# Kernel optimization log

Measured on AMD Instinct MI355X. Metric: run time of the kernel, lower is better.

## Reference

```python
import jax, jax.numpy as jnp
import numpy as np

B, S, D, DOUT = 16, 1024, 768, 256
TEMP = D ** 0.5


def setup_inputs() -> dict:
    key = jax.random.key(0)
    ks = jax.random.split(key, 16)
    emb = jax.random.normal(ks[0], (B, S, D), dtype=jnp.float32)
    mask = jax.random.randint(ks[1], (B, S), 0, 2, dtype=jnp.int32)
    scale = 0.02
    def lin(kw, kb, din, dout):
        return (jax.random.normal(kw, (din, dout), dtype=jnp.float32) * scale,
                jax.random.normal(kb, (dout,), dtype=jnp.float32) * scale)
    q_Wq, q_bq = lin(ks[2], ks[3], D, D)
    q_Wk, q_bk = lin(ks[4], ks[5], D, D)
    q_Wv, q_bv = lin(ks[6], ks[7], D, DOUT)
    d_Wq, d_bq = lin(ks[8], ks[9], D, D)
    d_Wk, d_bk = lin(ks[10], ks[11], D, D)
    d_Wv, d_bv = lin(ks[12], ks[13], D, DOUT)
    return {
        'emb': emb, 'mask': mask, 'is_query': 1,
        'query_Wq': q_Wq, 'query_bq': q_bq,
        'query_Wk': q_Wk, 'query_bk': q_bk,
        'query_Wv': q_Wv, 'query_bv': q_bv,
        'doc_Wq': d_Wq, 'doc_bq': d_bq,
        'doc_Wk': d_Wk, 'doc_bk': d_bk,
        'doc_Wv': d_Wv, 'doc_bv': d_bv,
    }


def reference(emb, mask, is_query,
              query_Wq, query_bq, query_Wk, query_bk, query_Wv, query_bv,
              doc_Wq, doc_bq, doc_Wk, doc_bk, doc_Wv, doc_bv):
    # is_query is a static Python int/bool selecting the projection set
    if is_query:
        Wq, bq, Wk, bk, Wv, bv = query_Wq, query_bq, query_Wk, query_bk, query_Wv, query_bv
    else:
        Wq, bq, Wk, bk, Wv, bv = doc_Wq, doc_bq, doc_Wk, doc_bk, doc_Wv, doc_bv
    q = jnp.einsum('bsd,de->bse', emb, Wq) + bq  # [B,S,D]
    k = jnp.einsum('bsd,de->bse', emb, Wk) + bk  # [B,S,D]
    v = jnp.einsum('bsd,de->bse', emb, Wv) + bv  # [B,S,DOUT]
    attn = jnp.einsum('bqd,bkd->bqk', q / TEMP, k)  # [B,S,S]
    attn = jnp.where(mask[:, None, :] == 0, jnp.float32(-1e9), attn)
    attn = jax.nn.softmax(attn, axis=-1)
    out = jnp.einsum('bqk,bkd->bqd', attn, v)  # [B,S,DOUT]
    return out, attn
```

## Files before the change

### kernel.cpp

```cpp
#include <hip/hip_runtime.h>
#include <hip/hip_bf16.h>

static constexpr float INV_TEMP = 0.03608439182435161f;

typedef __attribute__((ext_vector_type(8))) short bf16x8;
typedef __attribute__((ext_vector_type(4))) float f32x4;
typedef __attribute__((ext_vector_type(8))) unsigned short u16x8;
typedef __attribute__((ext_vector_type(4))) unsigned short u16x4;

__device__ __forceinline__ unsigned short f2bf(float f) {
  unsigned u = __float_as_uint(f);
  u += 0x7fffu + ((u >> 16) & 1u);
  return (unsigned short)(u >> 16);
}
__device__ __forceinline__ float bf2f(unsigned short h) {
  return __uint_as_float((unsigned)h << 16);
}

__device__ __forceinline__ void async_copy16(const void* g, void* lds) {
  __builtin_amdgcn_global_load_lds(
      (const __attribute__((address_space(1))) unsigned int*)g,
      (__attribute__((address_space(3))) unsigned int*)lds, 16, 0, 0);
}

__global__ __launch_bounds__(256) void pack_emb(const float* __restrict__ src,
                                                unsigned short* __restrict__ dst) {
  long i = ((long)blockIdx.x * 256 + threadIdx.x) * 8;
  float4 a = *(const float4*)(src + i);
  float4 b = *(const float4*)(src + i + 4);
  u16x8 v;
  v[0] = f2bf(a.x); v[1] = f2bf(a.y); v[2] = f2bf(a.z); v[3] = f2bf(a.w);
  v[4] = f2bf(b.x); v[5] = f2bf(b.y); v[6] = f2bf(b.z); v[7] = f2bf(b.w);
  *(u16x8*)(dst + i) = v;
}

__global__ __launch_bounds__(256) void pack_sel(
    const int* __restrict__ isq_p,
    const float* qWq, const float* qWk, const float* qWv, const float* qbv,
    const float* dWq, const float* dWk, const float* dWv, const float* dbv,
    unsigned short* __restrict__ Wq_bf,
    unsigned short* __restrict__ Wk_bf,
    unsigned short* __restrict__ WvT,
    float* __restrict__ bias_v) {
  const int b = blockIdx.x, t = threadIdx.x;
  const int isq = *isq_p;
  if (b < 1152) {
    const int which = b >= 576;
    const float* W = which ? (isq ? qWk : dWk) : (isq ? qWq : dWq);
    unsigned short* o = which ? Wk_bf : Wq_bf;
    const long i = ((long)(which ? b - 576 : b) * 256 + t) * 4;
    float4 x = *(const float4*)(W + i);
    u16x4 y; y[0] = f2bf(x.x); y[1] = f2bf(x.y); y[2] = f2bf(x.z); y[3] = f2bf(x.w);
    *(u16x4*)(o + i) = y;
  } else if (b < 1344) {
    const float* Wv = isq ? qWv : dWv;
    const long base = ((long)(b - 1152) * 256 + t) * 4;
#pragma unroll
    for (int j = 0; j < 4; ++j) {
      long o = base + j;
      int n = (int)(o / 768), d = (int)(o % 768);
      WvT[o] = f2bf(Wv[(long)d * 256 + n]);
    }
  } else {
    const float* bv = isq ? qbv : dbv;
    if (t < 256) bias_v[t] = bv[t];
  }
}

__global__ __launch_bounds__(256) void gemm_g(
    const unsigned short* __restrict__ Wk_bf,
    const unsigned short* __restrict__ Wq_bf,
    unsigned short* __restrict__ Gt) {
  __shared__ unsigned short Ab[2][64 * 32];
  __shared__ unsigned short Bb[2][64 * 32];
  const int tid = threadIdx.x, wid = tid >> 6, lane = tid & 63;
  const unsigned short* A = Wk_bf + (long)blockIdx.x * 64 * 768;
  const unsigned short* BT = Wq_bf + (long)blockIdx.y * 64 * 768;

  auto stage = [&](int buf, int kt) {
    const int e = tid * 8, row = e >> 5, col = e & 31;
    async_copy16(A + (long)row * 768 + kt * 32 + col, &Ab[buf][e]);
    async_copy16(BT + (long)row * 768 + kt * 32 + col, &Bb[buf][e]);
  };

  f32x4 acc[2][2] = {};
  stage(0, 0);
  __syncthreads();
  int buf = 0;
  const int wr = wid >> 1, wc = wid & 1;
  const int fr = lane & 15, fq = lane >> 4;
  for (int kt = 0; kt < 24; ++kt) {
    if (kt + 1 < 24) stage(buf ^ 1, kt + 1);
    const unsigned short* Ap = &Ab[buf][(wr * 32 + fr) * 32 + fq * 8];
    const unsigned short* Bp = &Bb[buf][(wc * 32 + fr) * 32 + fq * 8];
    bf16x8 a[2], b[2];
#pragma unroll
    for (int mi = 0; mi < 2; ++mi) a[mi] = *(const bf16x8*)(Ap + mi * 16 * 32);
#pragma unroll
    for (int ni = 0; ni < 2; ++ni) b[ni] = *(const bf16x8*)(Bp + ni * 16 * 32);
#pragma unroll
    for (int mi = 0; mi < 2; ++mi)
#pragma unroll
      for (int ni = 0; ni < 2; ++ni)
        acc[mi][ni] = __builtin_amdgcn_mfma_f32_16x16x32_bf16(a[mi], b[ni], acc[mi][ni], 0, 0, 0);
    __syncthreads();
    buf ^= 1;
  }
#pragma unroll
  for (int mi = 0; mi < 2; ++mi)
#pragma unroll
    for (int ni = 0; ni < 2; ++ni) {
      const long m = (long)blockIdx.x * 64 + wr * 32 + mi * 16 + fq * 4;
      const long n = (long)blockIdx.y * 64 + wc * 32 + ni * 16 + fr;
      f32x4 v = acc[mi][ni];
#pragma unroll
      for (int r = 0; r < 4; ++r) Gt[(m + r) * 768 + n] = f2bf(v[r]);
    }
}

__global__ __launch_bounds__(256) void uvc_fast(
    const int* __restrict__ isq_p,
    const float* qWq, const float* qbq, const float* qWk, const float* qbk,
    const float* dWq, const float* dbq, const float* dWk, const float* dbk,
    unsigned short* __restrict__ Gt, float* __restrict__ bias_t) {
  const int b = blockIdx.x, t = threadIdx.x;
  const int isq = *isq_p;
  const float* Wq = isq ? qWq : dWq;  const float* bq = isq ? qbq : dbq;
  const float* Wk = isq ? qWk : dWk;  const float* bk = isq ? qbk : dbk;
  __shared__ float red[256];
  if (b < 1536) {
    const int lo = (b < 768);
    const int d = lo ? b : b - 768;
    const float* W = lo ? Wq : Wk;
    const float* bvec = lo ? bk : bq;
    float s = 0.f;
#pragma unroll
    for (int i = 0; i < 3; ++i) {
      const int a = t + i * 256;
      s += W[(long)d * 768 + a] * bvec[a];
    }
    red[t] = s;
    __syncthreads();
    for (int off = 128; off; off >>= 1) {
      if (t < off) red[t] += red[t + off];
      __syncthreads();
    }
    if (t == 0) Gt[(long)(lo ? 768 : 769) * 768 + d] = f2bf(red[0]);
  } else {
    for (int i = t; i < 1024; i += 256) bias_t[i] = 0.f;
    float p = 0.f;
    for (int a = t; a < 768; a += 256) p += bq[a] * bk[a];
    red[t] = p;
    __syncthreads();
    for (int off = 128; off; off >>= 1) {
      if (t < off) red[t] += red[t + off];
      __syncthreads();
    }
    if (t == 0) bias_t[768] = red[0];
  }
}

__device__ __forceinline__ void k_loop_256(
    const unsigned short* __restrict__ Apan, long lda,
    const unsigned short* __restrict__ Bpan, long ldb,
    int nk, unsigned short* smem, f32x4 (&acc)[8][4]) {
  const int tid = threadIdx.x;
  const int wid = tid >> 6, lane = tid & 63;
  const int wr = wid >> 2, wc = wid & 3;
  const int fr = lane & 15, fq = lane >> 4;

  auto stage = [&](int tile, int mat, int ks, int buf) {
    const unsigned short* g = (mat ? Bpan : Apan) + (long)tile * 64 + ks * 32;
    const long ld = mat ? ldb : lda;
    unsigned short* d = smem + (((buf << 2) | (mat << 1) | ks) << 13);
#pragma unroll
    for (int i = 0; i < 2; ++i) {
      const int e = (tid + i * 512) * 8;
      const int row = e >> 5;
      const int sl = (e >> 3) & 3;
      const int ss = sl ^ ((row >> 1) & 3);
      async_copy16(g + (long)row * ld + ss * 8, d + e);
    }
  };

  const int fro = fr * 32 + ((fq ^ ((fr >> 1) & 3)) << 3);
  const int awo = fro + (wr * 128) * 32;
  const int bwo = fro + (wc * 64) * 32;

  stage(0, 0, 0, 0); stage(0, 1, 0, 0); stage(0, 0, 1, 0); stage(0, 1, 1, 0);
  if (nk > 1) {
    stage(1, 0, 0, 1); stage(1, 1, 1, 1);
    asm volatile("s_waitcnt vmcnt(4)" ::: "memory");
  } else {
    asm volatile("s_waitcnt vmcnt(0)" ::: "memory");
  }
  __builtin_amdgcn_sched_barrier(0);
  __builtin_amdgcn_s_barrier();

  for (int t = 0; t < nk; ++t) {
    const int p = t & 1;
    const unsigned short* A0 = smem + (((p << 2) | 0) << 13);
    const unsigned short* A1 = smem + (((p << 2) | 1) << 13);
    const unsigned short* B0 = smem + (((p << 2) | 2) << 13);
    const unsigned short* B1 = smem + (((p << 2) | 3) << 13);
    bf16x8 a[4], b[4];

#pragma unroll
    for (int m = 0; m < 4; ++m) a[m] = *(const bf16x8*)(A0 + awo + m * 512);
#pragma unroll
    for (int n = 0; n < 4; ++n) b[n] = *(const bf16x8*)(B0 + bwo + n * 512);
    if (t + 1 < nk) stage(t + 1, 0, 1, (t + 1) & 1);
    __builtin_amdgcn_s_barrier();
    asm volatile("s_waitcnt lgkmcnt(0)");
    __builtin_amdgcn_sched_barrier(0);
    __builtin_amdgcn_s_setprio(1);
#pragma unroll
    for (int m = 0; m < 4; ++m)
#pragma unroll
      for (int n = 0; n < 4; ++n)
        acc[m][n] = __builtin_amdgcn_mfma_f32_16x16x32_bf16(a[m], b[n], acc[m][n], 0, 0, 0);
    __builtin_amdgcn_s_setprio(0);
    __builtin_amdgcn_sched_barrier(0);
    __builtin_amdgcn_s_barrier();

#pragma unroll
    for (int m = 0; m < 4; ++m) a[m] = *(const bf16x8*)(A0 + awo + (4 + m) * 512);
    if (t + 1 < nk) stage(t + 1, 1, 0, (t + 1) & 1);
    __builtin_amdgcn_s_barrier();
    asm volatile("s_waitcnt lgkmcnt(0)");
    __builtin_amdgcn_sched_barrier(0);
    __builtin_amdgcn_s_setprio(1);
#pragma unroll
    for (int m = 0; m < 4; ++m)
#pragma unroll
      for (int n = 0; n < 4; ++n)
        acc[4 + m][n] = __builtin_amdgcn_mfma_f32_16x16x32_bf16(a[m], b[n], acc[4 + m][n], 0, 0, 0);
    __builtin_amdgcn_s_setprio(0);
    __builtin_amdgcn_sched_barrier(0);
    __builtin_amdgcn_s_barrier();

#pragma unroll
    for (int m = 0; m < 4; ++m) a[m] = *(const bf16x8*)(A1 + awo + m * 512);
#pragma unroll
    for (int n = 0; n < 4; ++n) b[n] = *(const bf16x8*)(B1 + bwo + n * 512);
    if (t + 2 < nk) stage(t + 2, 0, 0, p);
    __builtin_amdgcn_s_barrier();
    asm volatile("s_waitcnt lgkmcnt(0)");
    __builtin_amdgcn_sched_barrier(0);
    __builtin_amdgcn_s_setprio(1);
#pragma unroll
    for (int m = 0; m < 4; ++m)
#pragma unroll
      for (int n = 0; n < 4; ++n)
        acc[m][n] = __builtin_amdgcn_mfma_f32_16x16x32_bf16(a[m], b[n], acc[m][n], 0, 0, 0);
    __builtin_amdgcn_s_setprio(0);
    __builtin_amdgcn_sched_barrier(0);
    __builtin_amdgcn_s_barrier();

#pragma unroll
    for (int m = 0; m < 4; ++m) a[m] = *(const bf16x8*)(A1 + awo + (4 + m) * 512);
    if (t + 2 < nk) stage(t + 2, 1, 1, p);
    __builtin_amdgcn_s_barrier();
    asm volatile("s_waitcnt lgkmcnt(0)");
    __builtin_amdgcn_sched_barrier(0);
    __builtin_amdgcn_s_setprio(1);
#pragma unroll
    for (int m = 0; m < 4; ++m)
#pragma unroll
      for (int n = 0; n < 4; ++n)
        acc[4 + m][n] = __builtin_amdgcn_mfma_f32_16x16x32_bf16(a[m], b[n], acc[4 + m][n], 0, 0, 0);
    __builtin_amdgcn_s_setprio(0);
    if (t < nk - 2) {
      asm volatile("s_waitcnt vmcnt(4)" ::: "memory");
    } else if (t == nk - 2) {
      asm volatile("s_waitcnt vmcnt(0)" ::: "memory");
    }
    __builtin_amdgcn_sched_barrier(0);
    __builtin_amdgcn_s_barrier();
  }
}

__global__ __launch_bounds__(512, 2) void tproj256(
    const unsigned short* __restrict__ emb_bf,
    const unsigned short* __restrict__ Gt,
    const float* __restrict__ bias_t,
    unsigned short* __restrict__ T) {
  extern __shared__ unsigned short smem[];
  const int f = blockIdx.x;
  const int kx = f & 7, c = f >> 3;
  const long bx = 8 * kx + (c & 7);
  const long yb = c >> 3;
  const unsigned short* Apan = emb_bf + bx * 256 * 768;
  const unsigned short* Bpan = Gt + yb * 256 * 768;
  f32x4 acc[8][4];
#pragma unroll
  for (int m = 0; m < 8; ++m)
#pragma unroll
    for (int n = 0; n < 4; ++n) acc[m][n] = f32x4{0.f, 0.f, 0.f, 0.f};

  k_loop_256(Apan, 768, Bpan, 768, 12, smem, acc);

  const int wid = threadIdx.x >> 6, lane = threadIdx.x & 63;
  const int wr = wid >> 2, wc = wid & 3;
  const int fr = lane & 15, fq = lane >> 4;
#pragma unroll
  for (int m = 0; m < 8; ++m)
#pragma unroll
    for (int n = 0; n < 4; ++n) {
      const long mm = bx * 256 + wr * 128 + m * 16 + fq * 4;
      const long nn = yb * 256 + wc * 64 + n * 16 + fr;
      const float bb = bias_t[nn];
      f32x4 v = acc[m][n];
#pragma unroll
      for (int r = 0; r < 4; ++r) T[(mm + r) * 1024 + nn] = f2bf(v[r] + bb);
    }
}

__global__ __launch_bounds__(512, 2) void logits256(
    const unsigned short* __restrict__ T,
    const unsigned short* __restrict__ emb_bf,
    float* __restrict__ attn) {
  extern __shared__ unsigned short smem[];
  const int f = blockIdx.x;
  const int kx = f & 7, c = f >> 3;
  const int bz = 2 * kx + (c >> 4);
  const int inner = c & 15, bx = inner & 3, by = inner >> 2;
  const unsigned short* Tb = T + (long)bz * 1024 * 1024;
  const unsigned short* Apan = Tb + (long)bx * 256 * 1024;
  const unsigned short* Bpan = emb_bf + (long)bz * 1024 * 768 + (long)by * 256 * 768;
  f32x4 acc[8][4];
#pragma unroll
  for (int m = 0; m < 8; ++m)
#pragma unroll
    for (int n = 0; n < 4; ++n) acc[m][n] = f32x4{0.f, 0.f, 0.f, 0.f};

  k_loop_256(Apan, 1024, Bpan, 768, 12, smem, acc);

  const int wid = threadIdx.x >> 6, lane = threadIdx.x & 63;
  const int wr = wid >> 2, wc = wid & 3;
  const int fr = lane & 15, fq = lane >> 4;
  float* C = attn + (long)bz * 1024 * 1024;
#pragma unroll
  for (int m = 0; m < 8; ++m)
#pragma unroll
    for (int n = 0; n < 4; ++n) {
      const long mm = (long)bx * 256 + wr * 128 + m * 16 + fq * 4;
      const long nn = (long)by * 256 + wc * 64 + n * 16 + fr;
      const float cB = bf2f(Tb[nn * 1024 + 769]);
      f32x4 v = acc[m][n];
#pragma unroll
      for (int r = 0; r < 4; ++r) {
        const float rA = bf2f(Tb[(mm + r) * 1024 + 768]);
        C[(mm + r) * 1024 + nn] = (v[r] + rA + cB) * INV_TEMP;
      }
    }
}

__global__ __launch_bounds__(256) void gemm_vt(
    const unsigned short* __restrict__ WvT,
    const unsigned short* __restrict__ emb_bf,
    const float* __restrict__ bias_v,
    unsigned short* __restrict__ VT) {
  __shared__ unsigned short Ab[2][128 * 32];
  __shared__ unsigned short Bb[2][128 * 32];
  const int tid = threadIdx.x, wid = tid >> 6, lane = tid & 63;
  const unsigned short* A = WvT + (long)blockIdx.x * 128 * 768;
  const unsigned short* BT = emb_bf + (long)blockIdx.y * 128 * 768;
  const int srow = lane >> 2;
  const int skk = (lane & 3) * 8;

  auto stage = [&](int buf, int kt) {
    const unsigned short* As = A + (long)kt * 32;
    const unsigned short* Bs = BT + (long)kt * 32;
#pragma unroll
    for (int i = 0; i < 2; ++i) {
      int c = wid * 2 + i;
      async_copy16(As + (long)(c * 16 + srow) * 768 + skk, &Ab[buf][c * 512]);
      async_copy16(Bs + (long)(c * 16 + srow) * 768 + skk, &Bb[buf][c * 512]);
    }
  };

  f32x4 acc[4][4] = {};
  stage(0, 0);
  __syncthreads();
  int buf = 0;
  const int wr = wid >> 1, wc = wid & 1;
  const int fr = lane & 15, fq = lane >> 4;
  for (int kt = 0; kt < 24; ++kt) {
    if (kt + 1 < 24) stage(buf ^ 1, kt + 1);
    const unsigned short* Ap = &Ab[buf][(wr * 64 + fr) * 32 + fq * 8];
    const unsigned short* Bp = &Bb[buf][(wc * 64 + fr) * 32 + fq * 8];
    bf16x8 af[4], bfv[4];
#pragma unroll
    for (int mi = 0; mi < 4; ++mi) af[mi] = *(const bf16x8*)(Ap + mi * 16 * 32);
#pragma unroll
    for (int ni = 0; ni < 4; ++ni) bfv[ni] = *(const bf16x8*)(Bp + ni * 16 * 32);
#pragma unroll
    for (int mi = 0; mi < 4; ++mi)
#pragma unroll
      for (int ni = 0; ni < 4; ++ni)
        acc[mi][ni] = __builtin_amdgcn_mfma_f32_16x16x32_bf16(af[mi], bfv[ni], acc[mi][ni], 0, 0, 0);
    __syncthreads();
    buf ^= 1;
  }
#pragma unroll
  for (int mi = 0; mi < 4; ++mi)
#pragma unroll
    for (int ni = 0; ni < 4; ++ni) {
      const long m = (long)blockIdx.x * 128 + wr * 64 + mi * 16 + fq * 4;
      const long n = (long)blockIdx.y * 128 + wc * 64 + ni * 16 + fr;
      f32x4 v = acc[mi][ni];
#pragma unroll
      for (int r = 0; r < 4; ++r)
        VT[(m + r) * 16384 + n] = f2bf(v[r] + bias_v[m + r]);
    }
}

__global__ __launch_bounds__(256) void softmax_rows(float* __restrict__ attn,
                                                    const int* __restrict__ mask,
                                                    unsigned short* __restrict__ attn_bf) {
  const int row = blockIdx.x;
  const int b = row >> 10;
  float* p = attn + (long)row * 1024;
  const int tid = threadIdx.x, lane = tid & 63, wid = tid >> 6;
  float4 v = ((const float4*)p)[tid];
  int4 mk = ((const int4*)(mask + b * 1024))[tid];
  v.x = mk.x ? v.x : -1e9f;
  v.y = mk.y ? v.y : -1e9f;
  v.z = mk.z ? v.z : -1e9f;
  v.w = mk.w ? v.w : -1e9f;
  float mx = fmaxf(fmaxf(v.x, v.y), fmaxf(v.z, v.w));
#pragma unroll
  for (int off = 32; off; off >>= 1) mx = fmaxf(mx, __shfl_xor(mx, off));
  __shared__ float red[4];
  if (lane == 0) red[wid] = mx;
  __syncthreads();
  mx = fmaxf(fmaxf(red[0], red[1]), fmaxf(red[2], red[3]));
  float e0 = __expf(v.x - mx), e1 = __expf(v.y - mx);
  float e2 = __expf(v.z - mx), e3 = __expf(v.w - mx);
  float s = e0 + e1 + e2 + e3;
#pragma unroll
  for (int off = 32; off; off >>= 1) s += __shfl_xor(s, off);
  __shared__ float red2[4];
  if (lane == 0) red2[wid] = s;
  __syncthreads();
  s = red2[0] + red2[1] + red2[2] + red2[3];
  const float inv = 1.0f / s;
  float4 o;
  o.x = e0 * inv; o.y = e1 * inv; o.z = e2 * inv; o.w = e3 * inv;
  ((float4*)p)[tid] = o;
  u16x4 ob;
  ob[0] = f2bf(o.x); ob[1] = f2bf(o.y); ob[2] = f2bf(o.z); ob[3] = f2bf(o.w);
  *(u16x4*)(attn_bf + (long)row * 1024 + tid * 4) = ob;
}

__global__ __launch_bounds__(256) void gemm_pv(
    const unsigned short* __restrict__ attnbf,
    const unsigned short* __restrict__ VT,
    float* __restrict__ out) {
  __shared__ unsigned short Ab[2][128 * 32];
  __shared__ unsigned short Bb[2][64 * 32];
  const int tid = threadIdx.x, wid = tid >> 6, lane = tid & 63;
  const int bz = blockIdx.z;
  const unsigned short* A = attnbf + (long)bz * 1024 * 1024 + (long)blockIdx.x * 128 * 1024;
  const unsigned short* BT = VT + (long)bz * 1024 + (long)blockIdx.y * 64 * 16384;
  const int srow = lane >> 2;
  const int skk = (lane & 3) * 8;

  auto stage = [&](int buf, int kt) {
    const unsigned short* As = A + (long)kt * 32;
    const unsigned short* Bs = BT + (long)kt * 32;
#pragma unroll
    for (int i = 0; i < 2; ++i) {
      int c = wid * 2 + i;
      async_copy16(As + (long)(c * 16 + srow) * 1024 + skk, &Ab[buf][c * 512]);
    }
    async_copy16(Bs + (long)(wid * 16 + srow) * 16384 + skk, &Bb[buf][wid * 512]);
  };

  f32x4 acc[4][2] = {};
  stage(0, 0);
  __syncthreads();
  int buf = 0;
  const int wr = wid >> 1, wc = wid & 1;
  const int fr = lane & 15, fq = lane >> 4;
  for (int kt = 0; kt < 32; ++kt) {
    if (kt + 1 < 32) stage(buf ^ 1, kt + 1);
    const unsigned short* Ap = &Ab[buf][(wr * 64 + fr) * 32 + fq * 8];
    const unsigned short* Bp = &Bb[buf][(wc * 32 + fr) * 32 + fq * 8];
    bf16x8 af[4], bfv[2];
#pragma unroll
    for (int mi = 0; mi < 4; ++mi) af[mi] = *(const bf16x8*)(Ap + mi * 16 * 32);
#pragma unroll
    for (int ni = 0; ni < 2; ++ni) bfv[ni] = *(const bf16x8*)(Bp + ni * 16 * 32);
#pragma unroll
    for (int mi = 0; mi < 4; ++mi)
#pragma unroll
      for (int ni = 0; ni < 2; ++ni)
        acc[mi][ni] = __builtin_amdgcn_mfma_f32_16x16x32_bf16(af[mi], bfv[ni], acc[mi][ni], 0, 0, 0);
    __syncthreads();
    buf ^= 1;
  }

  float* C = out + (long)bz * 1024 * 256;
  const long m0 = (long)blockIdx.x * 128 + wr * 64;
  const long n0 = (long)blockIdx.y * 64 + wc * 32;
#pragma unroll
  for (int mi = 0; mi < 4; ++mi)
#pragma unroll
    for (int ni = 0; ni < 2; ++ni) {
      const long m = m0 + mi * 16 + fq * 4;
      const long n = n0 + ni * 16 + fr;
      f32x4 v = acc[mi][ni];
#pragma unroll
      for (int r = 0; r < 4; ++r) C[(m + r) * 256 + n] = v[r];
    }
}

extern "C" void kernel_launch(void* const* d_in, const int* in_sizes, int n_in,
                              void* d_out, int out_size, void* d_ws, size_t ws_size,
                              hipStream_t stream) {
  const float* emb = (const float*)d_in[0];
  const int* mask = (const int*)d_in[1];
  const int* isq = (const int*)d_in[2];
  const float* qWq = (const float*)d_in[3];  const float* qbq = (const float*)d_in[4];
  const float* qWk = (const float*)d_in[5];  const float* qbk = (const float*)d_in[6];
  const float* qWv = (const float*)d_in[7];  const float* qbv = (const float*)d_in[8];
  const float* dWq = (const float*)d_in[9];  const float* dbq = (const float*)d_in[10];
  const float* dWk = (const float*)d_in[11]; const float* dbk = (const float*)d_in[12];
  const float* dWv = (const float*)d_in[13]; const float* dbv = (const float*)d_in[14];

  char* ws = (char*)d_ws;
  unsigned short* emb_bf = (unsigned short*)ws;  ws += (size_t)16384 * 768 * 2;
  unsigned short* Wq_bf  = (unsigned short*)ws;  ws += (size_t)768 * 768 * 2;
  unsigned short* Wk_bf  = (unsigned short*)ws;  ws += (size_t)768 * 768 * 2;
  unsigned short* WvT    = (unsigned short*)ws;  ws += (size_t)256 * 768 * 2;
  unsigned short* Gt     = (unsigned short*)ws;  ws += (size_t)1024 * 768 * 2;
  float*          bias_v = (float*)ws;           ws += (size_t)256 * 4;
  float*          bias_t = (float*)ws;           ws += (size_t)1024 * 4;
  unsigned short* T      = (unsigned short*)ws;  ws += (size_t)16384 * 1024 * 2;
  unsigned short* VT     = (unsigned short*)ws;  ws += (size_t)256 * 16384 * 2;
  unsigned short* attnbf = (unsigned short*)ws;  ws += (size_t)16 * 1024 * 1024 * 2;

  float* out = (float*)d_out;
  float* attn = out + (size_t)16 * 1024 * 256;

  (void)hipFuncSetAttribute((const void*)&tproj256,
                            hipFuncAttributeMaxDynamicSharedMemorySize, 131072);
  (void)hipFuncSetAttribute((const void*)&logits256,
                            hipFuncAttributeMaxDynamicSharedMemorySize, 131072);

  hipLaunchKernelGGL(pack_emb, dim3(6144), dim3(256), 0, stream, emb, emb_bf);
  hipLaunchKernelGGL(pack_sel, dim3(1345), dim3(256), 0, stream, isq,
                     qWq, qWk, qWv, qbv, dWq, dWk, dWv, dbv, Wq_bf, Wk_bf, WvT, bias_v);
  hipLaunchKernelGGL(gemm_g, dim3(12, 12), dim3(256), 0, stream, Wk_bf, Wq_bf, Gt);
  hipLaunchKernelGGL(uvc_fast, dim3(1537), dim3(256), 0, stream, isq,
                     qWq, qbq, qWk, qbk, dWq, dbq, dWk, dbk, Gt, bias_t);
  hipLaunchKernelGGL(tproj256, dim3(256), dim3(512), 131072, stream,
                     emb_bf, Gt, bias_t, T);
  hipLaunchKernelGGL(gemm_vt, dim3(2, 128), dim3(256), 0, stream,
                     WvT, emb_bf, bias_v, VT);
  hipLaunchKernelGGL(logits256, dim3(256), dim3(512), 131072, stream,
                     T, emb_bf, attn);
  hipLaunchKernelGGL(softmax_rows, dim3(16384), dim3(256), 0, stream, attn, mask, attnbf);
  hipLaunchKernelGGL(gemm_pv, dim3(8, 4, 16), dim3(256), 0, stream, attnbf, VT, out);
}
```

Measured before the change: 171.9 us.

## Move rank-1 bias terms from padded T projection into extended V projection

The two bias-derived vectors (emb·Wq·bk and emb·Wk·bq) are now produced as extra rows of the V projection instead of as extra padded columns of the T = emb·G projection. T shrinks from 1024 to 768 columns, so the tproj GEMM launches 192 blocks instead of 256 and writes less data. The logits epilogue now reads the row and column bias vectors from the extended VT buffer. In exchange, gemm_vt grows from 2 to 3 row tiles, most of which is padding computed from uninitialized weight rows and never read.

```diff
diff --git a/kernel.cpp b/kernel.cpp
--- a/kernel.cpp
+++ b/kernel.cpp
@@ -40,7 +40,7 @@
     const float* dWq, const float* dWk, const float* dWv, const float* dbv,
     unsigned short* __restrict__ Wq_bf,
     unsigned short* __restrict__ Wk_bf,
-    unsigned short* __restrict__ WvT,
+    unsigned short* __restrict__ WvTe,
     float* __restrict__ bias_v) {
   const int b = blockIdx.x, t = threadIdx.x;
   const int isq = *isq_p;
@@ -59,7 +59,7 @@
     for (int j = 0; j < 4; ++j) {
       long o = base + j;
       int n = (int)(o / 768), d = (int)(o % 768);
-      WvT[o] = f2bf(Wv[(long)d * 256 + n]);
+      WvTe[o] = f2bf(Wv[(long)d * 256 + n]);
     }
   } else {
     const float* bv = isq ? qbv : dbv;
@@ -122,7 +122,7 @@
     const int* __restrict__ isq_p,
     const float* qWq, const float* qbq, const float* qWk, const float* qbk,
     const float* dWq, const float* dbq, const float* dWk, const float* dbk,
-    unsigned short* __restrict__ Gt, float* __restrict__ bias_t) {
+    unsigned short* __restrict__ WvTe, float* __restrict__ bias_v) {
   const int b = blockIdx.x, t = threadIdx.x;
   const int isq = *isq_p;
   const float* Wq = isq ? qWq : dWq;  const float* bq = isq ? qbq : dbq;
@@ -145,9 +145,9 @@
       if (t < off) red[t] += red[t + off];
       __syncthreads();
     }
-    if (t == 0) Gt[(long)(lo ? 768 : 769) * 768 + d] = f2bf(red[0]);
+    if (t == 0) WvTe[(long)(lo ? 256 : 257) * 768 + d] = f2bf(red[0]);
   } else {
-    for (int i = t; i < 1024; i += 256) bias_t[i] = 0.f;
+    if (t < 128) bias_v[256 + t] = 0.f;
     float p = 0.f;
     for (int a = t; a < 768; a += 256) p += bq[a] * bk[a];
     red[t] = p;
@@ -156,7 +156,7 @@
       if (t < off) red[t] += red[t + off];
       __syncthreads();
     }
-    if (t == 0) bias_t[768] = red[0];
+    if (t == 0) bias_v[256] = red[0];
   }
 }
 
@@ -283,7 +283,6 @@
 __global__ __launch_bounds__(512, 2) void tproj256(
     const unsigned short* __restrict__ emb_bf,
     const unsigned short* __restrict__ Gt,
-    const float* __restrict__ bias_t,
     unsigned short* __restrict__ T) {
   extern __shared__ unsigned short smem[];
   const int f = blockIdx.x;
@@ -309,24 +308,23 @@
     for (int n = 0; n < 4; ++n) {
       const long mm = bx * 256 + wr * 128 + m * 16 + fq * 4;
       const long nn = yb * 256 + wc * 64 + n * 16 + fr;
-      const float bb = bias_t[nn];
       f32x4 v = acc[m][n];
 #pragma unroll
-      for (int r = 0; r < 4; ++r) T[(mm + r) * 1024 + nn] = f2bf(v[r] + bb);
+      for (int r = 0; r < 4; ++r) T[(mm + r) * 768 + nn] = f2bf(v[r]);
     }
 }
 
 __global__ __launch_bounds__(512, 2) void logits256(
     const unsigned short* __restrict__ T,
     const unsigned short* __restrict__ emb_bf,
+    const unsigned short* __restrict__ VTe,
     float* __restrict__ attn) {
   extern __shared__ unsigned short smem[];
   const int f = blockIdx.x;
   const int kx = f & 7, c = f >> 3;
   const int bz = 2 * kx + (c >> 4);
   const int inner = c & 15, bx = inner & 3, by = inner >> 2;
-  const unsigned short* Tb = T + (long)bz * 1024 * 1024;
-  const unsigned short* Apan = Tb + (long)bx * 256 * 1024;
+  const unsigned short* Apan = T + (long)bz * 1024 * 768 + (long)bx * 256 * 768;
   const unsigned short* Bpan = emb_bf + (long)bz * 1024 * 768 + (long)by * 256 * 768;
   f32x4 acc[8][4];
 #pragma unroll
@@ -334,37 +332,39 @@
 #pragma unroll
     for (int n = 0; n < 4; ++n) acc[m][n] = f32x4{0.f, 0.f, 0.f, 0.f};
 
-  k_loop_256(Apan, 1024, Bpan, 768, 12, smem, acc);
+  k_loop_256(Apan, 768, Bpan, 768, 12, smem, acc);
 
   const int wid = threadIdx.x >> 6, lane = threadIdx.x & 63;
   const int wr = wid >> 2, wc = wid & 3;
   const int fr = lane & 15, fq = lane >> 4;
   float* C = attn + (long)bz * 1024 * 1024;
+  const unsigned short* rvec = VTe + (long)256 * 16384 + (long)bz * 1024;
+  const unsigned short* cvec = VTe + (long)257 * 16384 + (long)bz * 1024;
 #pragma unroll
   for (int m = 0; m < 8; ++m)
 #pragma unroll
     for (int n = 0; n < 4; ++n) {
       const long mm = (long)bx * 256 + wr * 128 + m * 16 + fq * 4;
       const long nn = (long)by * 256 + wc * 64 + n * 16 + fr;
-      const float cB = bf2f(Tb[nn * 1024 + 769]);
+      const float cB = bf2f(cvec[nn]);
       f32x4 v = acc[m][n];
 #pragma unroll
       for (int r = 0; r < 4; ++r) {
-        const float rA = bf2f(Tb[(mm + r) * 1024 + 768]);
+        const float rA = bf2f(rvec[mm + r]);
         C[(mm + r) * 1024 + nn] = (v[r] + rA + cB) * INV_TEMP;
       }
     }
 }
 
 __global__ __launch_bounds__(256) void gemm_vt(
-    const unsigned short* __restrict__ WvT,
+    const unsigned short* __restrict__ WvTe,
     const unsigned short* __restrict__ emb_bf,
     const float* __restrict__ bias_v,
-    unsigned short* __restrict__ VT) {
+    unsigned short* __restrict__ VTe) {
   __shared__ unsigned short Ab[2][128 * 32];
   __shared__ unsigned short Bb[2][128 * 32];
   const int tid = threadIdx.x, wid = tid >> 6, lane = tid & 63;
-  const unsigned short* A = WvT + (long)blockIdx.x * 128 * 768;
+  const unsigned short* A = WvTe + (long)blockIdx.x * 128 * 768;
   const unsigned short* BT = emb_bf + (long)blockIdx.y * 128 * 768;
   const int srow = lane >> 2;
   const int skk = (lane & 3) * 8;
@@ -412,7 +412,7 @@
       f32x4 v = acc[mi][ni];
 #pragma unroll
       for (int r = 0; r < 4; ++r)
-        VT[(m + r) * 16384 + n] = f2bf(v[r] + bias_v[m + r]);
+        VTe[(m + r) * 16384 + n] = f2bf(v[r] + bias_v[m + r]);
     }
 }
 
@@ -456,14 +456,14 @@
 
 __global__ __launch_bounds__(256) void gemm_pv(
     const unsigned short* __restrict__ attnbf,
-    const unsigned short* __restrict__ VT,
+    const unsigned short* __restrict__ VTe,
     float* __restrict__ out) {
   __shared__ unsigned short Ab[2][128 * 32];
   __shared__ unsigned short Bb[2][64 * 32];
   const int tid = threadIdx.x, wid = tid >> 6, lane = tid & 63;
   const int bz = blockIdx.z;
   const unsigned short* A = attnbf + (long)bz * 1024 * 1024 + (long)blockIdx.x * 128 * 1024;
-  const unsigned short* BT = VT + (long)bz * 1024 + (long)blockIdx.y * 64 * 16384;
+  const unsigned short* BT = VTe + (long)bz * 1024 + (long)blockIdx.y * 64 * 16384;
   const int srow = lane >> 2;
   const int skk = (lane & 3) * 8;
 
@@ -534,12 +534,11 @@
   unsigned short* emb_bf = (unsigned short*)ws;  ws += (size_t)16384 * 768 * 2;
   unsigned short* Wq_bf  = (unsigned short*)ws;  ws += (size_t)768 * 768 * 2;
   unsigned short* Wk_bf  = (unsigned short*)ws;  ws += (size_t)768 * 768 * 2;
-  unsigned short* WvT    = (unsigned short*)ws;  ws += (size_t)256 * 768 * 2;
-  unsigned short* Gt     = (unsigned short*)ws;  ws += (size_t)1024 * 768 * 2;
-  float*          bias_v = (float*)ws;           ws += (size_t)256 * 4;
-  float*          bias_t = (float*)ws;           ws += (size_t)1024 * 4;
-  unsigned short* T      = (unsigned short*)ws;  ws += (size_t)16384 * 1024 * 2;
-  unsigned short* VT     = (unsigned short*)ws;  ws += (size_t)256 * 16384 * 2;
+  unsigned short* WvTe   = (unsigned short*)ws;  ws += (size_t)384 * 768 * 2;
+  unsigned short* Gt     = (unsigned short*)ws;  ws += (size_t)768 * 768 * 2;
+  float*          bias_v = (float*)ws;           ws += (size_t)384 * 4;
+  unsigned short* T      = (unsigned short*)ws;  ws += (size_t)16384 * 768 * 2;
+  unsigned short* VTe    = (unsigned short*)ws;  ws += (size_t)384 * 16384 * 2;
   unsigned short* attnbf = (unsigned short*)ws;  ws += (size_t)16 * 1024 * 1024 * 2;
 
   float* out = (float*)d_out;
@@ -552,16 +551,15 @@
 
   hipLaunchKernelGGL(pack_emb, dim3(6144), dim3(256), 0, stream, emb, emb_bf);
   hipLaunchKernelGGL(pack_sel, dim3(1345), dim3(256), 0, stream, isq,
-                     qWq, qWk, qWv, qbv, dWq, dWk, dWv, dbv, Wq_bf, Wk_bf, WvT, bias_v);
+                     qWq, qWk, qWv, qbv, dWq, dWk, dWv, dbv, Wq_bf, Wk_bf, WvTe, bias_v);
   hipLaunchKernelGGL(gemm_g, dim3(12, 12), dim3(256), 0, stream, Wk_bf, Wq_bf, Gt);
   hipLaunchKernelGGL(uvc_fast, dim3(1537), dim3(256), 0, stream, isq,
-                     qWq, qbq, qWk, qbk, dWq, dbq, dWk, dbk, Gt, bias_t);
-  hipLaunchKernelGGL(tproj256, dim3(256), dim3(512), 131072, stream,
-                     emb_bf, Gt, bias_t, T);
-  hipLaunchKernelGGL(gemm_vt, dim3(2, 128), dim3(256), 0, stream,
-                     WvT, emb_bf, bias_v, VT);
+                     qWq, qbq, qWk, qbk, dWq, dbq, dWk, dbk, WvTe, bias_v);
+  hipLaunchKernelGGL(tproj256, dim3(192), dim3(512), 131072, stream, emb_bf, Gt, T);
+  hipLaunchKernelGGL(gemm_vt, dim3(3, 128), dim3(256), 0, stream,
+                     WvTe, emb_bf, bias_v, VTe);
   hipLaunchKernelGGL(logits256, dim3(256), dim3(512), 131072, stream,
-                     T, emb_bf, attn);
+                     T, emb_bf, VTe, attn);
   hipLaunchKernelGGL(softmax_rows, dim3(16384), dim3(256), 0, stream, attn, mask, attnbf);
-  hipLaunchKernelGGL(gemm_pv, dim3(8, 4, 16), dim3(256), 0, stream, attnbf, VT, out);
-}
+  hipLaunchKernelGGL(gemm_pv, dim3(8, 4, 16), dim3(256), 0, stream, attnbf, VTe, out);
+}
```

Result: no change. 169.8 us (-1.2%).
